# Optimization experiments

Hardware: AMD Instinct MI355X
Metric: run time of the kernel (lower is better)

Reference implementation:

```python
import jax, jax.numpy as jnp
import numpy as np

B, T, D = 2, 1024, 2048      # batch, seq, model dim
E, F, K = 64, 512, 4          # n_experts, expert hidden, top-k
S, HS = 2, 512 * 4            # shared experts, shared hidden = expert_dim * topk


def setup_inputs() -> dict:
    key = jax.random.key(0)
    ks = jax.random.split(key, 9)
    s = 0.02
    f32 = jnp.float32
    return {
        "x": jax.random.normal(ks[0], (B, T, D), f32),
        "router_w": jax.random.normal(ks[1], (D, E), f32) * s,
        "router_bias": jnp.zeros((E,), f32),
        "wg": jax.random.normal(ks[2], (E, D, F), f32) * s,
        "wu": jax.random.normal(ks[3], (E, D, F), f32) * s,
        "wd": jax.random.normal(ks[4], (E, F, D), f32) * s,
        "swg": jax.random.normal(ks[5], (S, D, HS), f32) * s,
        "swu": jax.random.normal(ks[6], (S, D, HS), f32) * s,
        "swd": jax.random.normal(ks[7], (S, HS, D), f32) * s,
    }


def reference(x, router_w, router_bias, wg, wu, wd, swg, swu, swd):
    b, t, d = x.shape
    flat = x.reshape(b * t, d)                      # [N, D]
    n = flat.shape[0]

    # Router: softmax scores, top-k selection on (logits + bias)
    logits = flat @ router_w                         # [N, E]
    scores = jax.nn.softmax(logits, axis=-1)
    _, topk_idx = jax.lax.top_k(logits + router_bias, K)          # [N, K]
    topk_scores = jnp.take_along_axis(scores, topk_idx, axis=-1)  # [N, K]
    topk_scores = topk_scores / topk_scores.sum(axis=-1, keepdims=True)

    # Dense combine weights: w[n, e] = normalized score if expert e selected else 0
    comb = jnp.zeros((n, E), dtype=flat.dtype).at[
        jnp.arange(n)[:, None], topk_idx].set(topk_scores)        # [N, E]

    # Routed experts (SwiGLU), computed densely and masked by combine weights
    g = jax.nn.silu(jnp.einsum('nd,edf->nef', flat, wg))          # [N, E, F]
    u = jnp.einsum('nd,edf->nef', flat, wu)                       # [N, E, F]
    routed = jnp.einsum('ne,nef,efd->nd', comb, g * u, wd)        # [N, D]

    # Shared experts (always active, summed)
    sg = jax.nn.silu(jnp.einsum('nd,sdh->nsh', flat, swg))        # [N, S, HS]
    su = jnp.einsum('nd,sdh->nsh', flat, swu)
    shared = jnp.einsum('nsh,shd->nd', sg * su, swd)              # [N, D]

    return (routed + shared).reshape(b, t, d)
```

## Files before the change

kernel.cpp:

```cpp
#include <hip/hip_runtime.h>
#include <hip/hip_bf16.h>

typedef __bf16 bf16x8 __attribute__((ext_vector_type(8)));
typedef float f32x4 __attribute__((ext_vector_type(4)));
typedef unsigned short u16x4 __attribute__((ext_vector_type(4)));
typedef unsigned short u16x8 __attribute__((ext_vector_type(8)));

#define DEVI __device__ __forceinline__

constexpr int N_TOK = 2048;
constexpr int DIM   = 2048;
constexpr int NEXP  = 64;
constexpr int FDIM  = 512;
constexpr int TOPK  = 4;
constexpr int NSH   = 2;
constexpr int HSH   = 2048;

DEVI unsigned short f2b(float f) {
  union { float fv; unsigned u; } v; v.fv = f;
  unsigned r = v.u + 0x7fffu + ((v.u >> 16) & 1u);
  return (unsigned short)(r >> 16);
}
DEVI float b2f(unsigned short h) {
  union { unsigned u; float f; } v; v.u = ((unsigned)h) << 16;
  return v.f;
}
DEVI void gll16(const void* g, void* l) {
  __builtin_amdgcn_global_load_lds((const __attribute__((address_space(1))) unsigned*)g,
                                   (__attribute__((address_space(3))) unsigned*)l, 16, 0, 0);
}
DEVI unsigned cvtpk(float lo, float hi) {
  unsigned r;
  asm("v_cvt_pk_bf16_f32 %0, %1, %2" : "=v"(r) : "v"(lo), "v"(hi));
  return r;
}
DEVI bf16x8 fragB(const float* base, int str) {
  union { unsigned u[4]; bf16x8 v; } r;
  #pragma unroll
  for (int p = 0; p < 4; ++p) r.u[p] = cvtpk(base[(2 * p) * str], base[(2 * p + 1) * str]);
  return r.v;
}

__global__ void cvt_x_kernel(const float* __restrict__ x, unsigned short* __restrict__ xb) {
  const size_t i = ((size_t)blockIdx.x * 256 + threadIdx.x) * 8;
  const float4 a = *reinterpret_cast<const float4*>(x + i);
  const float4 b = *reinterpret_cast<const float4*>(x + i + 4);
  u16x8 o;
  o[0] = f2b(a.x); o[1] = f2b(a.y); o[2] = f2b(a.z); o[3] = f2b(a.w);
  o[4] = f2b(b.x); o[5] = f2b(b.y); o[6] = f2b(b.z); o[7] = f2b(b.w);
  *reinterpret_cast<u16x8*>(xb + i) = o;
}

__global__ __launch_bounds__(256)
void tr_shared_kernel(const float* __restrict__ swu, const float* __restrict__ swg,
                      const float* __restrict__ swd, unsigned short* __restrict__ swuT,
                      unsigned short* __restrict__ swgT, unsigned short* __restrict__ swdT) {
  __shared__ float Lf[64][68];
  const int tid = threadIdx.x;
  const int r0 = blockIdx.x * 64, c0 = blockIdx.y * 64;
  const int z = blockIdx.z, mat = z >> 1;
  const size_t soff = (size_t)(z & 1) * DIM * HSH;
  const float* in = (mat == 0 ? swu : mat == 1 ? swg : swd) + soff;
  unsigned short* ot = (mat == 0 ? swuT : mat == 1 ? swgT : swdT) + soff;
  #pragma unroll
  for (int j = 0; j < 4; ++j) {
    const int idx = j * 1024 + tid * 4;
    const int row = idx >> 6, col = idx & 63;
    const float4 v = *reinterpret_cast<const float4*>(in + (size_t)(r0 + row) * 2048 + c0 + col);
    *reinterpret_cast<float4*>(&Lf[row][col]) = v;
  }
  __syncthreads();
  #pragma unroll
  for (int j = 0; j < 4; ++j) {
    const int idx = j * 1024 + tid * 4;
    const int orow = idx >> 6, ocol = idx & 63;
    u16x4 o;
    o[0] = f2b(Lf[ocol][orow]);     o[1] = f2b(Lf[ocol + 1][orow]);
    o[2] = f2b(Lf[ocol + 2][orow]); o[3] = f2b(Lf[ocol + 3][orow]);
    *reinterpret_cast<u16x4*>(ot + (size_t)(c0 + orow) * 2048 + r0 + ocol) = o;
  }
}

__global__ __launch_bounds__(256)
void router_kernel(const float* __restrict__ x, const float* __restrict__ rw,
                   const float* __restrict__ rb, int* __restrict__ cnt,
                   int* __restrict__ listTok, float* __restrict__ listW,
                   int* __restrict__ tokEP) {
  __shared__ float Lx[8][128];
  const int tid = threadIdx.x;
  const int lane = tid & 63;
  const int wave = tid >> 6;
  const int tokBase = blockIdx.x * 8;

  float acc0 = 0.f, acc1 = 0.f;
  for (int dc = 0; dc < DIM; dc += 128) {
    __syncthreads();
    {
      const int idx = tid * 4;
      const int row = idx >> 7, col = idx & 127;
      *reinterpret_cast<float4*>(&Lx[row][col]) =
          *reinterpret_cast<const float4*>(x + (size_t)(tokBase + row) * DIM + dc + col);
    }
    __syncthreads();
    #pragma unroll 16
    for (int dd = 0; dd < 128; ++dd) {
      const float r = rw[(size_t)(dc + dd) * NEXP + lane];
      acc0 = fmaf(Lx[wave * 2 + 0][dd], r, acc0);
      acc1 = fmaf(Lx[wave * 2 + 1][dd], r, acc1);
    }
  }

  const float bias = rb[lane];
  #pragma unroll
  for (int t = 0; t < 2; ++t) {
    const float v = (t == 0) ? acc0 : acc1;
    const int token = tokBase + wave * 2 + t;
    float m = v;
    #pragma unroll
    for (int o = 32; o > 0; o >>= 1) m = fmaxf(m, __shfl_xor(m, o));
    const float p = expf(v - m);
    float ss = p;
    #pragma unroll
    for (int o = 32; o > 0; o >>= 1) ss += __shfl_xor(ss, o);
    const float score = p / ss;
    float cur = v + bias;
    float wk[TOPK]; int ik[TOPK]; float wsum = 0.f;
    #pragma unroll
    for (int k = 0; k < TOPK; ++k) {
      float tm = cur;
      #pragma unroll
      for (int o = 32; o > 0; o >>= 1) tm = fmaxf(tm, __shfl_xor(tm, o));
      const unsigned long long msk = __ballot(cur == tm);
      const int sel = (int)__builtin_ctzll(msk);
      const float w = __shfl(score, sel);
      wk[k] = w; ik[k] = sel; wsum += w;
      if (lane == sel) cur = -3.4e38f;
    }
    if (lane < TOPK) {
      const int e = ik[lane];
      const float w = wk[lane] / wsum;
      const int slot = atomicAdd(&cnt[e], 1);
      listTok[(size_t)e * N_TOK + slot] = token;
      listW[(size_t)e * N_TOK + slot] = w;
      tokEP[token * TOPK + lane] = (e << 16) | slot;
    }
  }
}

__global__ void scan_kernel(const int* __restrict__ cnt, int* __restrict__ off) {
  if (threadIdx.x == 0) {
    int s = 0;
    for (int e = 0; e < NEXP; ++e) { off[e] = s; s += cnt[e]; }
  }
}

__global__ __launch_bounds__(256, 4)
void up_shared(const unsigned short* __restrict__ xb,
               const unsigned short* __restrict__ WuT, const unsigned short* __restrict__ WgT,
               unsigned short* __restrict__ H) {
  constexpr int NT = DIM / 64;
  const int tid = threadIdx.x;
  const int f0 = blockIdx.x * 64;
  const int s  = blockIdx.y;
  const int m0 = blockIdx.z * 128;

  __shared__ __align__(16) unsigned short Al[8][128][8];
  __shared__ __align__(16) unsigned short BuL[8][64][8];
  __shared__ __align__(16) unsigned short BgL[8][64][8];

  const int wid = tid >> 6, l = tid & 63;
  const int lc = l & 15, hi = l >> 4;

  const unsigned short* pa0 = xb + (size_t)(m0 + l) * DIM;
  const unsigned short* pa1 = xb + (size_t)(m0 + 64 + l) * DIM;
  const unsigned short* pbu = WuT + (size_t)s * HSH * DIM + (size_t)(f0 + l) * DIM;
  const unsigned short* pbg = WgT + (size_t)s * HSH * DIM + (size_t)(f0 + l) * DIM;

  f32x4 aU[2][4], aG[2][4];
  #pragma unroll
  for (int i = 0; i < 2; ++i)
    #pragma unroll
    for (int j = 0; j < 4; ++j) { aU[i][j] = f32x4{0,0,0,0}; aG[i][j] = f32x4{0,0,0,0}; }

  for (int g = 0; g < NT; ++g) {
    const int d0 = g * 64;
    #pragma unroll
    for (int i = 0; i < 4; ++i) {
      const int idx = wid * 4 + i;
      const int p = idx >> 1, hf = idx & 1;
      gll16((hf ? pa1 : pa0) + d0 + p * 8, &Al[p][hf * 64][0]);
    }
    #pragma unroll
    for (int i = 0; i < 2; ++i) {
      const int p = wid * 2 + i;
      gll16(pbu + d0 + p * 8, &BuL[p][0][0]);
      gll16(pbg + d0 + p * 8, &BgL[p][0][0]);
    }
    __syncthreads();
    #pragma unroll
    for (int ks = 0; ks < 2; ++ks) {
      bf16x8 af[2], bu[4], bg[4];
      #pragma unroll
      for (int mi = 0; mi < 2; ++mi)
        af[mi] = *reinterpret_cast<const bf16x8*>(&Al[ks * 4 + hi][wid * 32 + mi * 16 + lc][0]);
      #pragma unroll
      for (int ni = 0; ni < 4; ++ni) {
        bu[ni] = *reinterpret_cast<const bf16x8*>(&BuL[ks * 4 + hi][ni * 16 + lc][0]);
        bg[ni] = *reinterpret_cast<const bf16x8*>(&BgL[ks * 4 + hi][ni * 16 + lc][0]);
      }
      #pragma unroll
      for (int mi = 0; mi < 2; ++mi)
        #pragma unroll
        for (int ni = 0; ni < 4; ++ni) {
          aU[mi][ni] = __builtin_amdgcn_mfma_f32_16x16x32_bf16(af[mi], bu[ni], aU[mi][ni], 0, 0, 0);
          aG[mi][ni] = __builtin_amdgcn_mfma_f32_16x16x32_bf16(af[mi], bg[ni], aG[mi][ni], 0, 0, 0);
        }
    }
    __syncthreads();
  }

  #pragma unroll
  for (int mi = 0; mi < 2; ++mi)
    #pragma unroll
    for (int ni = 0; ni < 4; ++ni)
      #pragma unroll
      for (int r2 = 0; r2 < 4; ++r2) {
        const int row = wid * 32 + mi * 16 + hi * 4 + r2;
        const int col = f0 + ni * 16 + lc;
        const float g = aG[mi][ni][r2], u = aU[mi][ni][r2];
        H[((size_t)s * N_TOK + m0 + row) * HSH + col] = f2b((g / (1.f + __expf(-g))) * u);
      }
}

__global__ __launch_bounds__(256, 4)
void down_shared(const unsigned short* __restrict__ Hs, const unsigned short* __restrict__ swdT,
                 unsigned short* __restrict__ shP) {
  constexpr int NT = 16;
  const int tid = threadIdx.x;
  const int x0 = blockIdx.x * 128;
  const int kc = blockIdx.y;
  const int m0 = blockIdx.z * 128;
  const int seg = kc >> 1;
  const int kb = (kc & 1) * 1024;

  __shared__ __align__(16) unsigned short Al[8][128][8];
  __shared__ __align__(16) unsigned short Bl[8][128][8];

  const int wid = tid >> 6, l = tid & 63;
  const int lc = l & 15, hi = l >> 4;

  const unsigned short* pa0 = Hs + ((size_t)seg * N_TOK + m0 + l) * HSH + kb;
  const unsigned short* pa1 = Hs + ((size_t)seg * N_TOK + m0 + 64 + l) * HSH + kb;
  const unsigned short* pb0 = swdT + (size_t)seg * HSH * DIM + (size_t)(x0 + l) * HSH + kb;
  const unsigned short* pb1 = swdT + (size_t)seg * HSH * DIM + (size_t)(x0 + 64 + l) * HSH + kb;

  f32x4 acc[2][8];
  #pragma unroll
  for (int i = 0; i < 2; ++i)
    #pragma unroll
    for (int j = 0; j < 8; ++j) acc[i][j] = f32x4{0,0,0,0};

  for (int g = 0; g < NT; ++g) {
    const int d0 = g * 64;
    #pragma unroll
    for (int i = 0; i < 4; ++i) {
      const int idx = wid * 4 + i;
      const int p = idx >> 1, hf = idx & 1;
      gll16((hf ? pa1 : pa0) + d0 + p * 8, &Al[p][hf * 64][0]);
      gll16((hf ? pb1 : pb0) + d0 + p * 8, &Bl[p][hf * 64][0]);
    }
    __syncthreads();
    #pragma unroll
    for (int ks = 0; ks < 2; ++ks) {
      bf16x8 af[2], bq[8];
      #pragma unroll
      for (int mi = 0; mi < 2; ++mi)
        af[mi] = *reinterpret_cast<const bf16x8*>(&Al[ks * 4 + hi][wid * 32 + mi * 16 + lc][0]);
      #pragma unroll
      for (int ni = 0; ni < 8; ++ni)
        bq[ni] = *reinterpret_cast<const bf16x8*>(&Bl[ks * 4 + hi][ni * 16 + lc][0]);
      #pragma unroll
      for (int mi = 0; mi < 2; ++mi)
        #pragma unroll
        for (int ni = 0; ni < 8; ++ni)
          acc[mi][ni] = __builtin_amdgcn_mfma_f32_16x16x32_bf16(af[mi], bq[ni], acc[mi][ni], 0, 0, 0);
    }
    __syncthreads();
  }

  unsigned short* pout = shP + (size_t)kc * N_TOK * DIM;
  #pragma unroll
  for (int mi = 0; mi < 2; ++mi)
    #pragma unroll
    for (int ni = 0; ni < 8; ++ni)
      #pragma unroll
      for (int r2 = 0; r2 < 4; ++r2) {
        const int row = wid * 32 + mi * 16 + hi * 4 + r2;
        const int col = x0 + ni * 16 + lc;
        pout[(size_t)(m0 + row) * DIM + col] = f2b(acc[mi][ni][r2]);
      }
}

__global__ __launch_bounds__(256, 2)
void up_routed(const unsigned short* __restrict__ xb,
               const float* __restrict__ Wu, const float* __restrict__ Wg,
               const int* __restrict__ cnt, const int* __restrict__ off,
               const int* __restrict__ listTok, const float* __restrict__ listW,
               unsigned short* __restrict__ H) {
  constexpr int NT = DIM / 64;
  const int tid = threadIdx.x;
  const int f0 = blockIdx.x * 64;
  const int e  = blockIdx.y;
  const int m0 = blockIdx.z * 256;
  const int c = cnt[e];
  if (m0 >= c) return;
  const int rc = min(256, c - m0);
  const int rowbase = off[e] + m0;

  __shared__ __align__(16) unsigned short Al[8][256][8];
  __shared__ __align__(16) float Bfu[64][64];
  __shared__ __align__(16) float Bfg[64][64];
  __shared__ float wSs[256];

  wSs[tid] = (m0 + tid < c) ? listW[(size_t)e * N_TOK + m0 + tid] : 0.f;

  const int wid = tid >> 6, l = tid & 63;
  const int lc = l & 15, hi = l >> 4;

  const unsigned short* pa[4];
  #pragma unroll
  for (int j = 0; j < 4; ++j) {
    const int tok = listTok[(size_t)e * N_TOK + min(m0 + j * 64 + l, c - 1)];
    pa[j] = xb + (size_t)tok * DIM;
  }
  const float* pwu = Wu + (size_t)e * DIM * FDIM + (size_t)(l >> 4) * FDIM + f0 + (l & 15) * 4;
  const float* pwg = Wg + (size_t)e * DIM * FDIM + (size_t)(l >> 4) * FDIM + f0 + (l & 15) * 4;

  f32x4 aU[4][4], aG[4][4];
  #pragma unroll
  for (int i = 0; i < 4; ++i)
    #pragma unroll
    for (int j = 0; j < 4; ++j) { aU[i][j] = f32x4{0,0,0,0}; aG[i][j] = f32x4{0,0,0,0}; }

  for (int g = 0; g < NT; ++g) {
    const int d0 = g * 64;
    #pragma unroll
    for (int i = 0; i < 8; ++i) {
      const int idx = wid * 8 + i;
      const int p = idx >> 2, j = idx & 3;
      gll16(pa[j] + d0 + p * 8, &Al[p][j * 64][0]);
    }
    #pragma unroll
    for (int i = 0; i < 4; ++i) {
      const int krow = (wid * 4 + i) * 4;
      gll16(pwu + (size_t)(d0 + krow) * FDIM, &Bfu[krow][0]);
      gll16(pwg + (size_t)(d0 + krow) * FDIM, &Bfg[krow][0]);
    }
    __syncthreads();
    #pragma unroll
    for (int ks = 0; ks < 2; ++ks) {
      bf16x8 af[4];
      #pragma unroll
      for (int mi = 0; mi < 4; ++mi)
        af[mi] = *reinterpret_cast<const bf16x8*>(&Al[ks * 4 + hi][wid * 64 + mi * 16 + lc][0]);
      #pragma unroll
      for (int ni = 0; ni < 4; ++ni) {
        const bf16x8 bu = fragB(&Bfu[ks * 32 + hi * 8][ni * 16 + lc], 64);
        const bf16x8 bg = fragB(&Bfg[ks * 32 + hi * 8][ni * 16 + lc], 64);
        #pragma unroll
        for (int mi = 0; mi < 4; ++mi) {
          aU[mi][ni] = __builtin_amdgcn_mfma_f32_16x16x32_bf16(af[mi], bu, aU[mi][ni], 0, 0, 0);
          aG[mi][ni] = __builtin_amdgcn_mfma_f32_16x16x32_bf16(af[mi], bg, aG[mi][ni], 0, 0, 0);
        }
      }
    }
    __syncthreads();
  }

  #pragma unroll
  for (int mi = 0; mi < 4; ++mi)
    #pragma unroll
    for (int ni = 0; ni < 4; ++ni)
      #pragma unroll
      for (int r2 = 0; r2 < 4; ++r2) {
        const int row = wid * 64 + mi * 16 + hi * 4 + r2;
        if (row < rc) {
          const int col = f0 + ni * 16 + lc;
          const float g = aG[mi][ni][r2], u = aU[mi][ni][r2];
          const float h = (g / (1.f + __expf(-g))) * u * wSs[row];
          H[(size_t)(rowbase + row) * FDIM + col] = f2b(h);
        }
      }
}

__global__ __launch_bounds__(256, 2)
void down_routed(const unsigned short* __restrict__ Hr, const float* __restrict__ wd,
                 const int* __restrict__ cnt, const int* __restrict__ off,
                 unsigned short* __restrict__ P) {
  constexpr int NT = FDIM / 64;
  const int tid = threadIdx.x;
  const int x0 = blockIdx.x * 128;
  const int e  = blockIdx.y;
  const int m0 = blockIdx.z * 256;
  const int c = cnt[e];
  if (m0 >= c) return;
  const int rc = min(256, c - m0);
  const int rowbase = off[e] + m0;

  __shared__ __align__(16) unsigned short Al[8][256][8];
  __shared__ __align__(16) float Bf[64][128];

  const int wid = tid >> 6, l = tid & 63;
  const int lc = l & 15, hi = l >> 4;

  const unsigned short* pa[4];
  #pragma unroll
  for (int j = 0; j < 4; ++j)
    pa[j] = Hr + (size_t)(rowbase + min(j * 64 + l, c - m0 - 1)) * FDIM;

  const float* pwd = wd + (size_t)e * FDIM * DIM + (size_t)(l >> 5) * DIM + x0 + (l & 31) * 4;

  f32x4 acc[4][8];
  #pragma unroll
  for (int i = 0; i < 4; ++i)
    #pragma unroll
    for (int j = 0; j < 8; ++j) acc[i][j] = f32x4{0,0,0,0};

  for (int g = 0; g < NT; ++g) {
    const int d0 = g * 64;
    #pragma unroll
    for (int i = 0; i < 8; ++i) {
      const int idx = wid * 8 + i;
      const int p = idx >> 2, j = idx & 3;
      gll16(pa[j] + d0 + p * 8, &Al[p][j * 64][0]);
    }
    #pragma unroll
    for (int i = 0; i < 8; ++i) {
      const int krow = (wid * 8 + i) * 2;
      gll16(pwd + (size_t)(d0 + krow) * DIM, &Bf[krow][0]);
    }
    __syncthreads();
    #pragma unroll
    for (int ks = 0; ks < 2; ++ks) {
      bf16x8 af[4];
      #pragma unroll
      for (int mi = 0; mi < 4; ++mi)
        af[mi] = *reinterpret_cast<const bf16x8*>(&Al[ks * 4 + hi][wid * 64 + mi * 16 + lc][0]);
      #pragma unroll
      for (int ni = 0; ni < 8; ++ni) {
        const bf16x8 bq = fragB(&Bf[ks * 32 + hi * 8][ni * 16 + lc], 128);
        #pragma unroll
        for (int mi = 0; mi < 4; ++mi)
          acc[mi][ni] = __builtin_amdgcn_mfma_f32_16x16x32_bf16(af[mi], bq, acc[mi][ni], 0, 0, 0);
      }
    }
    __syncthreads();
  }

  #pragma unroll
  for (int mi = 0; mi < 4; ++mi)
    #pragma unroll
    for (int ni = 0; ni < 8; ++ni)
      #pragma unroll
      for (int r2 = 0; r2 < 4; ++r2) {
        const int row = wid * 64 + mi * 16 + hi * 4 + r2;
        if (row < rc) {
          const int col = x0 + ni * 16 + lc;
          P[(size_t)(rowbase + row) * DIM + col] = f2b(acc[mi][ni][r2]);
        }
      }
}

__global__ __launch_bounds__(256)
void combine_kernel(const int* __restrict__ tokEP, const int* __restrict__ off,
                    const unsigned short* __restrict__ P, const unsigned short* __restrict__ shP,
                    float* __restrict__ out) {
  const int n = blockIdx.x;
  const int tid = threadIdx.x;
  int rows[4];
  #pragma unroll
  for (int k = 0; k < TOPK; ++k) {
    const int ep = tokEP[n * TOPK + k];
    rows[k] = off[ep >> 16] + (ep & 0xffff);
  }
  const int cc = tid * 8;
  float4 o0 = {0, 0, 0, 0}, o1 = {0, 0, 0, 0};
  #pragma unroll
  for (int k = 0; k < TOPK; ++k) {
    const u16x8 v = *reinterpret_cast<const u16x8*>(P + (size_t)rows[k] * DIM + cc);
    o0.x += b2f(v[0]); o0.y += b2f(v[1]); o0.z += b2f(v[2]); o0.w += b2f(v[3]);
    o1.x += b2f(v[4]); o1.y += b2f(v[5]); o1.z += b2f(v[6]); o1.w += b2f(v[7]);
  }
  #pragma unroll
  for (int j = 0; j < 4; ++j) {
    const u16x8 v = *reinterpret_cast<const u16x8*>(shP + ((size_t)j * N_TOK + n) * DIM + cc);
    o0.x += b2f(v[0]); o0.y += b2f(v[1]); o0.z += b2f(v[2]); o0.w += b2f(v[3]);
    o1.x += b2f(v[4]); o1.y += b2f(v[5]); o1.z += b2f(v[6]); o1.w += b2f(v[7]);
  }
  float* po = out + (size_t)n * DIM + cc;
  *reinterpret_cast<float4*>(po) = o0;
  *reinterpret_cast<float4*>(po + 4) = o1;
}

extern "C" void kernel_launch(void* const* d_in, const int* in_sizes, int n_in,
                              void* d_out, int out_size, void* d_ws, size_t ws_size,
                              hipStream_t stream) {
  const float* x   = (const float*)d_in[0];
  const float* rw  = (const float*)d_in[1];
  const float* rb  = (const float*)d_in[2];
  const float* wg  = (const float*)d_in[3];
  const float* wu  = (const float*)d_in[4];
  const float* wd  = (const float*)d_in[5];
  const float* swg = (const float*)d_in[6];
  const float* swu = (const float*)d_in[7];
  const float* swd = (const float*)d_in[8];
  float* out = (float*)d_out;
  char* ws = (char*)d_ws;

  int* cnt = (int*)ws;
  int* off = (int*)(ws + 256);
  int* tokEP = (int*)(ws + 4096);
  int* listTok = (int*)(ws + 64 * 1024);
  float* listW = (float*)(ws + 576 * 1024);
  unsigned short* xb   = (unsigned short*)(ws + (size_t) 2 * 1024 * 1024);
  unsigned short* Hr   = (unsigned short*)(ws + (size_t)10 * 1024 * 1024);
  unsigned short* Hs   = (unsigned short*)(ws + (size_t)18 * 1024 * 1024);
  unsigned short* swuT = (unsigned short*)(ws + (size_t)34 * 1024 * 1024);
  unsigned short* swgT = (unsigned short*)(ws + (size_t)50 * 1024 * 1024);
  unsigned short* swdT = (unsigned short*)(ws + (size_t)66 * 1024 * 1024);
  unsigned short* P    = (unsigned short*)(ws + (size_t)82 * 1024 * 1024);
  unsigned short* shP  = swuT;

  hipMemsetAsync(cnt, 0, NEXP * sizeof(int), stream);
  cvt_x_kernel<<<(N_TOK * DIM) / (256 * 8), 256, 0, stream>>>(x, xb);
  router_kernel<<<N_TOK / 8, 256, 0, stream>>>(x, rw, rb, cnt, listTok, listW, tokEP);
  scan_kernel<<<1, 64, 0, stream>>>(cnt, off);
  tr_shared_kernel<<<dim3(32, 32, 6), 256, 0, stream>>>(swu, swg, swd, swuT, swgT, swdT);

  up_shared<<<dim3(HSH / 64, NSH, N_TOK / 128), 256, 0, stream>>>(xb, swuT, swgT, Hs);
  up_routed<<<dim3(FDIM / 64, NEXP, 8), 256, 0, stream>>>(xb, wu, wg, cnt, off, listTok, listW, Hr);
  down_shared<<<dim3(DIM / 128, 4, N_TOK / 128), 256, 0, stream>>>(Hs, swdT, shP);
  down_routed<<<dim3(DIM / 128, NEXP, 8), 256, 0, stream>>>(Hr, wd, cnt, off, P);
  combine_kernel<<<N_TOK, 256, 0, stream>>>(tokEP, off, P, shP, out);
}
```

Measured before the change: 576.6 us.

## Drop shared-weight transpose pass; load fp32 weights directly in shared-expert GEMMs

Removes the separate transpose-and-convert kernel for the shared expert weights. The shared up and down GEMMs now stream the original fp32 weights into LDS and convert them to bf16 fragments on the fly with fragB. This avoids one full read, bf16 write and re-read of about 48M weight elements. The cost is twice the global and LDS traffic per B tile, strided scalar LDS reads plus convert instructions in the inner loop, and lower occupancy bounds (3 instead of 4) because the LDS tiles are larger.

```diff
diff --git a/kernel.cpp b/kernel.cpp
--- a/kernel.cpp
+++ b/kernel.cpp
@@ -49,36 +49,6 @@
   o[0] = f2b(a.x); o[1] = f2b(a.y); o[2] = f2b(a.z); o[3] = f2b(a.w);
   o[4] = f2b(b.x); o[5] = f2b(b.y); o[6] = f2b(b.z); o[7] = f2b(b.w);
   *reinterpret_cast<u16x8*>(xb + i) = o;
-}
-
-__global__ __launch_bounds__(256)
-void tr_shared_kernel(const float* __restrict__ swu, const float* __restrict__ swg,
-                      const float* __restrict__ swd, unsigned short* __restrict__ swuT,
-                      unsigned short* __restrict__ swgT, unsigned short* __restrict__ swdT) {
-  __shared__ float Lf[64][68];
-  const int tid = threadIdx.x;
-  const int r0 = blockIdx.x * 64, c0 = blockIdx.y * 64;
-  const int z = blockIdx.z, mat = z >> 1;
-  const size_t soff = (size_t)(z & 1) * DIM * HSH;
-  const float* in = (mat == 0 ? swu : mat == 1 ? swg : swd) + soff;
-  unsigned short* ot = (mat == 0 ? swuT : mat == 1 ? swgT : swdT) + soff;
-  #pragma unroll
-  for (int j = 0; j < 4; ++j) {
-    const int idx = j * 1024 + tid * 4;
-    const int row = idx >> 6, col = idx & 63;
-    const float4 v = *reinterpret_cast<const float4*>(in + (size_t)(r0 + row) * 2048 + c0 + col);
-    *reinterpret_cast<float4*>(&Lf[row][col]) = v;
-  }
-  __syncthreads();
-  #pragma unroll
-  for (int j = 0; j < 4; ++j) {
-    const int idx = j * 1024 + tid * 4;
-    const int orow = idx >> 6, ocol = idx & 63;
-    u16x4 o;
-    o[0] = f2b(Lf[ocol][orow]);     o[1] = f2b(Lf[ocol + 1][orow]);
-    o[2] = f2b(Lf[ocol + 2][orow]); o[3] = f2b(Lf[ocol + 3][orow]);
-    *reinterpret_cast<u16x4*>(ot + (size_t)(c0 + orow) * 2048 + r0 + ocol) = o;
-  }
 }
 
 __global__ __launch_bounds__(256)
@@ -154,9 +124,9 @@
   }
 }
 
-__global__ __launch_bounds__(256, 4)
+__global__ __launch_bounds__(256, 3)
 void up_shared(const unsigned short* __restrict__ xb,
-               const unsigned short* __restrict__ WuT, const unsigned short* __restrict__ WgT,
+               const float* __restrict__ swu, const float* __restrict__ swg,
                unsigned short* __restrict__ H) {
   constexpr int NT = DIM / 64;
   const int tid = threadIdx.x;
@@ -165,16 +135,16 @@
   const int m0 = blockIdx.z * 128;
 
   __shared__ __align__(16) unsigned short Al[8][128][8];
-  __shared__ __align__(16) unsigned short BuL[8][64][8];
-  __shared__ __align__(16) unsigned short BgL[8][64][8];
+  __shared__ __align__(16) float Bfu[64][64];
+  __shared__ __align__(16) float Bfg[64][64];
 
   const int wid = tid >> 6, l = tid & 63;
   const int lc = l & 15, hi = l >> 4;
 
   const unsigned short* pa0 = xb + (size_t)(m0 + l) * DIM;
   const unsigned short* pa1 = xb + (size_t)(m0 + 64 + l) * DIM;
-  const unsigned short* pbu = WuT + (size_t)s * HSH * DIM + (size_t)(f0 + l) * DIM;
-  const unsigned short* pbg = WgT + (size_t)s * HSH * DIM + (size_t)(f0 + l) * DIM;
+  const float* pwu = swu + (size_t)s * DIM * HSH + (size_t)(l >> 4) * HSH + f0 + (l & 15) * 4;
+  const float* pwg = swg + (size_t)s * DIM * HSH + (size_t)(l >> 4) * HSH + f0 + (l & 15) * 4;
 
   f32x4 aU[2][4], aG[2][4];
   #pragma unroll
@@ -191,30 +161,28 @@
       gll16((hf ? pa1 : pa0) + d0 + p * 8, &Al[p][hf * 64][0]);
     }
     #pragma unroll
-    for (int i = 0; i < 2; ++i) {
-      const int p = wid * 2 + i;
-      gll16(pbu + d0 + p * 8, &BuL[p][0][0]);
-      gll16(pbg + d0 + p * 8, &BgL[p][0][0]);
+    for (int i = 0; i < 4; ++i) {
+      const int krow = (wid * 4 + i) * 4;
+      gll16(pwu + (size_t)(d0 + krow) * HSH, &Bfu[krow][0]);
+      gll16(pwg + (size_t)(d0 + krow) * HSH, &Bfg[krow][0]);
     }
     __syncthreads();
     #pragma unroll
     for (int ks = 0; ks < 2; ++ks) {
-      bf16x8 af[2], bu[4], bg[4];
+      bf16x8 af[2];
       #pragma unroll
       for (int mi = 0; mi < 2; ++mi)
         af[mi] = *reinterpret_cast<const bf16x8*>(&Al[ks * 4 + hi][wid * 32 + mi * 16 + lc][0]);
       #pragma unroll
       for (int ni = 0; ni < 4; ++ni) {
-        bu[ni] = *reinterpret_cast<const bf16x8*>(&BuL[ks * 4 + hi][ni * 16 + lc][0]);
-        bg[ni] = *reinterpret_cast<const bf16x8*>(&BgL[ks * 4 + hi][ni * 16 + lc][0]);
-      }
-      #pragma unroll
-      for (int mi = 0; mi < 2; ++mi)
+        const bf16x8 bu = fragB(&Bfu[ks * 32 + hi * 8][ni * 16 + lc], 64);
+        const bf16x8 bg = fragB(&Bfg[ks * 32 + hi * 8][ni * 16 + lc], 64);
         #pragma unroll
-        for (int ni = 0; ni < 4; ++ni) {
-          aU[mi][ni] = __builtin_amdgcn_mfma_f32_16x16x32_bf16(af[mi], bu[ni], aU[mi][ni], 0, 0, 0);
-          aG[mi][ni] = __builtin_amdgcn_mfma_f32_16x16x32_bf16(af[mi], bg[ni], aG[mi][ni], 0, 0, 0);
+        for (int mi = 0; mi < 2; ++mi) {
+          aU[mi][ni] = __builtin_amdgcn_mfma_f32_16x16x32_bf16(af[mi], bu, aU[mi][ni], 0, 0, 0);
+          aG[mi][ni] = __builtin_amdgcn_mfma_f32_16x16x32_bf16(af[mi], bg, aG[mi][ni], 0, 0, 0);
         }
+      }
     }
     __syncthreads();
   }
@@ -232,8 +200,8 @@
       }
 }
 
-__global__ __launch_bounds__(256, 4)
-void down_shared(const unsigned short* __restrict__ Hs, const unsigned short* __restrict__ swdT,
+__global__ __launch_bounds__(256, 3)
+void down_shared(const unsigned short* __restrict__ Hs, const float* __restrict__ swd,
                  unsigned short* __restrict__ shP) {
   constexpr int NT = 16;
   const int tid = threadIdx.x;
@@ -244,15 +212,14 @@
   const int kb = (kc & 1) * 1024;
 
   __shared__ __align__(16) unsigned short Al[8][128][8];
-  __shared__ __align__(16) unsigned short Bl[8][128][8];
+  __shared__ __align__(16) float Bf[64][128];
 
   const int wid = tid >> 6, l = tid & 63;
   const int lc = l & 15, hi = l >> 4;
 
   const unsigned short* pa0 = Hs + ((size_t)seg * N_TOK + m0 + l) * HSH + kb;
   const unsigned short* pa1 = Hs + ((size_t)seg * N_TOK + m0 + 64 + l) * HSH + kb;
-  const unsigned short* pb0 = swdT + (size_t)seg * HSH * DIM + (size_t)(x0 + l) * HSH + kb;
-  const unsigned short* pb1 = swdT + (size_t)seg * HSH * DIM + (size_t)(x0 + 64 + l) * HSH + kb;
+  const float* pwd = swd + (size_t)seg * HSH * DIM + (size_t)(kb + (l >> 5)) * DIM + x0 + (l & 31) * 4;
 
   f32x4 acc[2][8];
   #pragma unroll
@@ -267,23 +234,26 @@
       const int idx = wid * 4 + i;
       const int p = idx >> 1, hf = idx & 1;
       gll16((hf ? pa1 : pa0) + d0 + p * 8, &Al[p][hf * 64][0]);
-      gll16((hf ? pb1 : pb0) + d0 + p * 8, &Bl[p][hf * 64][0]);
+    }
+    #pragma unroll
+    for (int i = 0; i < 8; ++i) {
+      const int krow = (wid * 8 + i) * 2;
+      gll16(pwd + (size_t)(d0 + krow) * DIM, &Bf[krow][0]);
     }
     __syncthreads();
     #pragma unroll
     for (int ks = 0; ks < 2; ++ks) {
-      bf16x8 af[2], bq[8];
+      bf16x8 af[2];
       #pragma unroll
       for (int mi = 0; mi < 2; ++mi)
         af[mi] = *reinterpret_cast<const bf16x8*>(&Al[ks * 4 + hi][wid * 32 + mi * 16 + lc][0]);
       #pragma unroll
-      for (int ni = 0; ni < 8; ++ni)
-        bq[ni] = *reinterpret_cast<const bf16x8*>(&Bl[ks * 4 + hi][ni * 16 + lc][0]);
-      #pragma unroll
-      for (int mi = 0; mi < 2; ++mi)
+      for (int ni = 0; ni < 8; ++ni) {
+        const bf16x8 bq = fragB(&Bf[ks * 32 + hi * 8][ni * 16 + lc], 128);
         #pragma unroll
-        for (int ni = 0; ni < 8; ++ni)
-          acc[mi][ni] = __builtin_amdgcn_mfma_f32_16x16x32_bf16(af[mi], bq[ni], acc[mi][ni], 0, 0, 0);
+        for (int mi = 0; mi < 2; ++mi)
+          acc[mi][ni] = __builtin_amdgcn_mfma_f32_16x16x32_bf16(af[mi], bq, acc[mi][ni], 0, 0, 0);
+      }
     }
     __syncthreads();
   }
@@ -522,24 +492,20 @@
   int* tokEP = (int*)(ws + 4096);
   int* listTok = (int*)(ws + 64 * 1024);
   float* listW = (float*)(ws + 576 * 1024);
-  unsigned short* xb   = (unsigned short*)(ws + (size_t) 2 * 1024 * 1024);
-  unsigned short* Hr   = (unsigned short*)(ws + (size_t)10 * 1024 * 1024);
-  unsigned short* Hs   = (unsigned short*)(ws + (size_t)18 * 1024 * 1024);
-  unsigned short* swuT = (unsigned short*)(ws + (size_t)34 * 1024 * 1024);
-  unsigned short* swgT = (unsigned short*)(ws + (size_t)50 * 1024 * 1024);
-  unsigned short* swdT = (unsigned short*)(ws + (size_t)66 * 1024 * 1024);
-  unsigned short* P    = (unsigned short*)(ws + (size_t)82 * 1024 * 1024);
-  unsigned short* shP  = swuT;
+  unsigned short* xb  = (unsigned short*)(ws + (size_t) 2 * 1024 * 1024);
+  unsigned short* Hr  = (unsigned short*)(ws + (size_t)10 * 1024 * 1024);
+  unsigned short* Hs  = (unsigned short*)(ws + (size_t)18 * 1024 * 1024);
+  unsigned short* P   = (unsigned short*)(ws + (size_t)34 * 1024 * 1024);
+  unsigned short* shP = (unsigned short*)(ws + (size_t)66 * 1024 * 1024);
 
   hipMemsetAsync(cnt, 0, NEXP * sizeof(int), stream);
   cvt_x_kernel<<<(N_TOK * DIM) / (256 * 8), 256, 0, stream>>>(x, xb);
   router_kernel<<<N_TOK / 8, 256, 0, stream>>>(x, rw, rb, cnt, listTok, listW, tokEP);
   scan_kernel<<<1, 64, 0, stream>>>(cnt, off);
-  tr_shared_kernel<<<dim3(32, 32, 6), 256, 0, stream>>>(swu, swg, swd, swuT, swgT, swdT);
-
-  up_shared<<<dim3(HSH / 64, NSH, N_TOK / 128), 256, 0, stream>>>(xb, swuT, swgT, Hs);
+
+  up_shared<<<dim3(HSH / 64, NSH, N_TOK / 128), 256, 0, stream>>>(xb, swu, swg, Hs);
   up_routed<<<dim3(FDIM / 64, NEXP, 8), 256, 0, stream>>>(xb, wu, wg, cnt, off, listTok, listW, Hr);
-  down_shared<<<dim3(DIM / 128, 4, N_TOK / 128), 256, 0, stream>>>(Hs, swdT, shP);
+  down_shared<<<dim3(DIM / 128, 4, N_TOK / 128), 256, 0, stream>>>(Hs, swd, shP);
   down_routed<<<dim3(DIM / 128, NEXP, 8), 256, 0, stream>>>(Hr, wd, cnt, off, P);
   combine_kernel<<<N_TOK, 256, 0, stream>>>(tokEP, off, P, shP, out);
 }
```

Result: slower. 609.3 us (+5.7%).

## Split routed up-projection into two passes and shrink down-projection tiles

Applied to the files above, without the earlier changes.

The fused gate/up routed kernel becomes a templated kernel launched twice. The first pass writes the up projection to H as bf16, and the second computes the gate, reads u back from H and applies SiLU and the routing weight. The down-projection tile narrows from 128 to 64 columns, and both kernels raise launch bounds to 3 blocks per SU to cut accumulator registers and LDS and raise occupancy. In exchange the token gather from x is read twice, H takes an extra bf16 round trip through global memory (the u value is rounded before the product), and there are more blocks and one extra launch.

```diff
diff --git a/kernel.cpp b/kernel.cpp
--- a/kernel.cpp
+++ b/kernel.cpp
@@ -301,9 +301,9 @@
       }
 }
 
-__global__ __launch_bounds__(256, 2)
-void up_routed(const unsigned short* __restrict__ xb,
-               const float* __restrict__ Wu, const float* __restrict__ Wg,
+template<bool GPASS>
+__global__ __launch_bounds__(256, 3)
+void up_routed(const unsigned short* __restrict__ xb, const float* __restrict__ W,
                const int* __restrict__ cnt, const int* __restrict__ off,
                const int* __restrict__ listTok, const float* __restrict__ listW,
                unsigned short* __restrict__ H) {
@@ -318,11 +318,10 @@
   const int rowbase = off[e] + m0;
 
   __shared__ __align__(16) unsigned short Al[8][256][8];
-  __shared__ __align__(16) float Bfu[64][64];
-  __shared__ __align__(16) float Bfg[64][64];
+  __shared__ __align__(16) float Bf[64][64];
   __shared__ float wSs[256];
 
-  wSs[tid] = (m0 + tid < c) ? listW[(size_t)e * N_TOK + m0 + tid] : 0.f;
+  if (GPASS) wSs[tid] = (m0 + tid < c) ? listW[(size_t)e * N_TOK + m0 + tid] : 0.f;
 
   const int wid = tid >> 6, l = tid & 63;
   const int lc = l & 15, hi = l >> 4;
@@ -333,14 +332,13 @@
     const int tok = listTok[(size_t)e * N_TOK + min(m0 + j * 64 + l, c - 1)];
     pa[j] = xb + (size_t)tok * DIM;
   }
-  const float* pwu = Wu + (size_t)e * DIM * FDIM + (size_t)(l >> 4) * FDIM + f0 + (l & 15) * 4;
-  const float* pwg = Wg + (size_t)e * DIM * FDIM + (size_t)(l >> 4) * FDIM + f0 + (l & 15) * 4;
-
-  f32x4 aU[4][4], aG[4][4];
+  const float* pw = W + (size_t)e * DIM * FDIM + (size_t)(l >> 4) * FDIM + f0 + (l & 15) * 4;
+
+  f32x4 acc[4][4];
   #pragma unroll
   for (int i = 0; i < 4; ++i)
     #pragma unroll
-    for (int j = 0; j < 4; ++j) { aU[i][j] = f32x4{0,0,0,0}; aG[i][j] = f32x4{0,0,0,0}; }
+    for (int j = 0; j < 4; ++j) acc[i][j] = f32x4{0,0,0,0};
 
   for (int g = 0; g < NT; ++g) {
     const int d0 = g * 64;
@@ -353,8 +351,7 @@
     #pragma unroll
     for (int i = 0; i < 4; ++i) {
       const int krow = (wid * 4 + i) * 4;
-      gll16(pwu + (size_t)(d0 + krow) * FDIM, &Bfu[krow][0]);
-      gll16(pwg + (size_t)(d0 + krow) * FDIM, &Bfg[krow][0]);
+      gll16(pw + (size_t)(d0 + krow) * FDIM, &Bf[krow][0]);
     }
     __syncthreads();
     #pragma unroll
@@ -365,13 +362,10 @@
         af[mi] = *reinterpret_cast<const bf16x8*>(&Al[ks * 4 + hi][wid * 64 + mi * 16 + lc][0]);
       #pragma unroll
       for (int ni = 0; ni < 4; ++ni) {
-        const bf16x8 bu = fragB(&Bfu[ks * 32 + hi * 8][ni * 16 + lc], 64);
-        const bf16x8 bg = fragB(&Bfg[ks * 32 + hi * 8][ni * 16 + lc], 64);
+        const bf16x8 bq = fragB(&Bf[ks * 32 + hi * 8][ni * 16 + lc], 64);
         #pragma unroll
-        for (int mi = 0; mi < 4; ++mi) {
-          aU[mi][ni] = __builtin_amdgcn_mfma_f32_16x16x32_bf16(af[mi], bu, aU[mi][ni], 0, 0, 0);
-          aG[mi][ni] = __builtin_amdgcn_mfma_f32_16x16x32_bf16(af[mi], bg, aG[mi][ni], 0, 0, 0);
-        }
+        for (int mi = 0; mi < 4; ++mi)
+          acc[mi][ni] = __builtin_amdgcn_mfma_f32_16x16x32_bf16(af[mi], bq, acc[mi][ni], 0, 0, 0);
       }
     }
     __syncthreads();
@@ -386,20 +380,25 @@
         const int row = wid * 64 + mi * 16 + hi * 4 + r2;
         if (row < rc) {
           const int col = f0 + ni * 16 + lc;
-          const float g = aG[mi][ni][r2], u = aU[mi][ni][r2];
-          const float h = (g / (1.f + __expf(-g))) * u * wSs[row];
-          H[(size_t)(rowbase + row) * FDIM + col] = f2b(h);
+          const size_t idx = (size_t)(rowbase + row) * FDIM + col;
+          const float v = acc[mi][ni][r2];
+          if (GPASS) {
+            const float u = b2f(H[idx]);
+            H[idx] = f2b((v / (1.f + __expf(-v))) * u * wSs[row]);
+          } else {
+            H[idx] = f2b(v);
+          }
         }
       }
 }
 
-__global__ __launch_bounds__(256, 2)
+__global__ __launch_bounds__(256, 3)
 void down_routed(const unsigned short* __restrict__ Hr, const float* __restrict__ wd,
                  const int* __restrict__ cnt, const int* __restrict__ off,
                  unsigned short* __restrict__ P) {
   constexpr int NT = FDIM / 64;
   const int tid = threadIdx.x;
-  const int x0 = blockIdx.x * 128;
+  const int x0 = blockIdx.x * 64;
   const int e  = blockIdx.y;
   const int m0 = blockIdx.z * 256;
   const int c = cnt[e];
@@ -408,7 +407,7 @@
   const int rowbase = off[e] + m0;
 
   __shared__ __align__(16) unsigned short Al[8][256][8];
-  __shared__ __align__(16) float Bf[64][128];
+  __shared__ __align__(16) float Bf[64][64];
 
   const int wid = tid >> 6, l = tid & 63;
   const int lc = l & 15, hi = l >> 4;
@@ -418,13 +417,13 @@
   for (int j = 0; j < 4; ++j)
     pa[j] = Hr + (size_t)(rowbase + min(j * 64 + l, c - m0 - 1)) * FDIM;
 
-  const float* pwd = wd + (size_t)e * FDIM * DIM + (size_t)(l >> 5) * DIM + x0 + (l & 31) * 4;
-
-  f32x4 acc[4][8];
+  const float* pwd = wd + (size_t)e * FDIM * DIM + (size_t)(l >> 4) * DIM + x0 + (l & 15) * 4;
+
+  f32x4 acc[4][4];
   #pragma unroll
   for (int i = 0; i < 4; ++i)
     #pragma unroll
-    for (int j = 0; j < 8; ++j) acc[i][j] = f32x4{0,0,0,0};
+    for (int j = 0; j < 4; ++j) acc[i][j] = f32x4{0,0,0,0};
 
   for (int g = 0; g < NT; ++g) {
     const int d0 = g * 64;
@@ -435,8 +434,8 @@
       gll16(pa[j] + d0 + p * 8, &Al[p][j * 64][0]);
     }
     #pragma unroll
-    for (int i = 0; i < 8; ++i) {
-      const int krow = (wid * 8 + i) * 2;
+    for (int i = 0; i < 4; ++i) {
+      const int krow = (wid * 4 + i) * 4;
       gll16(pwd + (size_t)(d0 + krow) * DIM, &Bf[krow][0]);
     }
     __syncthreads();
@@ -447,8 +446,8 @@
       for (int mi = 0; mi < 4; ++mi)
         af[mi] = *reinterpret_cast<const bf16x8*>(&Al[ks * 4 + hi][wid * 64 + mi * 16 + lc][0]);
       #pragma unroll
-      for (int ni = 0; ni < 8; ++ni) {
-        const bf16x8 bq = fragB(&Bf[ks * 32 + hi * 8][ni * 16 + lc], 128);
+      for (int ni = 0; ni < 4; ++ni) {
+        const bf16x8 bq = fragB(&Bf[ks * 32 + hi * 8][ni * 16 + lc], 64);
         #pragma unroll
         for (int mi = 0; mi < 4; ++mi)
           acc[mi][ni] = __builtin_amdgcn_mfma_f32_16x16x32_bf16(af[mi], bq, acc[mi][ni], 0, 0, 0);
@@ -460,7 +459,7 @@
   #pragma unroll
   for (int mi = 0; mi < 4; ++mi)
     #pragma unroll
-    for (int ni = 0; ni < 8; ++ni)
+    for (int ni = 0; ni < 4; ++ni)
       #pragma unroll
       for (int r2 = 0; r2 < 4; ++r2) {
         const int row = wid * 64 + mi * 16 + hi * 4 + r2;
@@ -538,8 +537,9 @@
   tr_shared_kernel<<<dim3(32, 32, 6), 256, 0, stream>>>(swu, swg, swd, swuT, swgT, swdT);
 
   up_shared<<<dim3(HSH / 64, NSH, N_TOK / 128), 256, 0, stream>>>(xb, swuT, swgT, Hs);
-  up_routed<<<dim3(FDIM / 64, NEXP, 8), 256, 0, stream>>>(xb, wu, wg, cnt, off, listTok, listW, Hr);
+  up_routed<false><<<dim3(FDIM / 64, NEXP, 8), 256, 0, stream>>>(xb, wu, cnt, off, listTok, listW, Hr);
+  up_routed<true ><<<dim3(FDIM / 64, NEXP, 8), 256, 0, stream>>>(xb, wg, cnt, off, listTok, listW, Hr);
   down_shared<<<dim3(DIM / 128, 4, N_TOK / 128), 256, 0, stream>>>(Hs, swdT, shP);
-  down_routed<<<dim3(DIM / 128, NEXP, 8), 256, 0, stream>>>(Hr, wd, cnt, off, P);
+  down_routed<<<dim3(DIM / 64, NEXP, 8), 256, 0, stream>>>(Hr, wd, cnt, off, P);
   combine_kernel<<<N_TOK, 256, 0, stream>>>(tokEP, off, P, shP, out);
 }
```

After: 643.3 us. +11.6%, slower.

## Double-buffer LDS staging in routed up-projection kernel with half-depth K tiles

Applied to the files above, without the earlier changes.

The routed gate/up GEMM kernel now uses two LDS buffers of 32-wide K tiles instead of one 64-wide tile. The next tile's global-to-LDS loads are issued before the current tile's MFMAs, so memory latency can overlap with compute. Total shared-memory footprint stays the same. The trade-off is twice as many loop iterations and barriers, and each barrier still waits for the in-flight prefetch, which limits how much overlap is possible.

```diff
diff --git a/kernel.cpp b/kernel.cpp
--- a/kernel.cpp
+++ b/kernel.cpp
@@ -307,7 +307,7 @@
                const int* __restrict__ cnt, const int* __restrict__ off,
                const int* __restrict__ listTok, const float* __restrict__ listW,
                unsigned short* __restrict__ H) {
-  constexpr int NT = DIM / 64;
+  constexpr int NT = DIM / 32;
   const int tid = threadIdx.x;
   const int f0 = blockIdx.x * 64;
   const int e  = blockIdx.y;
@@ -317,9 +317,9 @@
   const int rc = min(256, c - m0);
   const int rowbase = off[e] + m0;
 
-  __shared__ __align__(16) unsigned short Al[8][256][8];
-  __shared__ __align__(16) float Bfu[64][64];
-  __shared__ __align__(16) float Bfg[64][64];
+  __shared__ __align__(16) unsigned short Al[2][4][256][8];
+  __shared__ __align__(16) float Bfu[2][32][64];
+  __shared__ __align__(16) float Bfg[2][32][64];
   __shared__ float wSs[256];
 
   wSs[tid] = (m0 + tid < c) ? listW[(size_t)e * N_TOK + m0 + tid] : 0.f;
@@ -342,36 +342,37 @@
     #pragma unroll
     for (int j = 0; j < 4; ++j) { aU[i][j] = f32x4{0,0,0,0}; aG[i][j] = f32x4{0,0,0,0}; }
 
+  auto stage = [&](int g, int b) {
+    const int d0 = g * 32;
+    #pragma unroll
+    for (int j = 0; j < 4; ++j)
+      gll16(pa[j] + d0 + wid * 8, &Al[b][wid][j * 64][0]);
+    #pragma unroll
+    for (int i = 0; i < 2; ++i) {
+      const int krow = (wid * 2 + i) * 4;
+      gll16(pwu + (size_t)(d0 + krow) * FDIM, &Bfu[b][krow][0]);
+      gll16(pwg + (size_t)(d0 + krow) * FDIM, &Bfg[b][krow][0]);
+    }
+  };
+
+  stage(0, 0);
+  __syncthreads();
+
   for (int g = 0; g < NT; ++g) {
-    const int d0 = g * 64;
-    #pragma unroll
-    for (int i = 0; i < 8; ++i) {
-      const int idx = wid * 8 + i;
-      const int p = idx >> 2, j = idx & 3;
-      gll16(pa[j] + d0 + p * 8, &Al[p][j * 64][0]);
-    }
-    #pragma unroll
-    for (int i = 0; i < 4; ++i) {
-      const int krow = (wid * 4 + i) * 4;
-      gll16(pwu + (size_t)(d0 + krow) * FDIM, &Bfu[krow][0]);
-      gll16(pwg + (size_t)(d0 + krow) * FDIM, &Bfg[krow][0]);
-    }
-    __syncthreads();
-    #pragma unroll
-    for (int ks = 0; ks < 2; ++ks) {
-      bf16x8 af[4];
-      #pragma unroll
-      for (int mi = 0; mi < 4; ++mi)
-        af[mi] = *reinterpret_cast<const bf16x8*>(&Al[ks * 4 + hi][wid * 64 + mi * 16 + lc][0]);
-      #pragma unroll
-      for (int ni = 0; ni < 4; ++ni) {
-        const bf16x8 bu = fragB(&Bfu[ks * 32 + hi * 8][ni * 16 + lc], 64);
-        const bf16x8 bg = fragB(&Bfg[ks * 32 + hi * 8][ni * 16 + lc], 64);
-        #pragma unroll
-        for (int mi = 0; mi < 4; ++mi) {
-          aU[mi][ni] = __builtin_amdgcn_mfma_f32_16x16x32_bf16(af[mi], bu, aU[mi][ni], 0, 0, 0);
-          aG[mi][ni] = __builtin_amdgcn_mfma_f32_16x16x32_bf16(af[mi], bg, aG[mi][ni], 0, 0, 0);
-        }
+    const int b = g & 1;
+    if (g + 1 < NT) stage(g + 1, b ^ 1);
+    bf16x8 af[4];
+    #pragma unroll
+    for (int mi = 0; mi < 4; ++mi)
+      af[mi] = *reinterpret_cast<const bf16x8*>(&Al[b][hi][wid * 64 + mi * 16 + lc][0]);
+    #pragma unroll
+    for (int ni = 0; ni < 4; ++ni) {
+      const bf16x8 bu = fragB(&Bfu[b][hi * 8][ni * 16 + lc], 64);
+      const bf16x8 bg = fragB(&Bfg[b][hi * 8][ni * 16 + lc], 64);
+      #pragma unroll
+      for (int mi = 0; mi < 4; ++mi) {
+        aU[mi][ni] = __builtin_amdgcn_mfma_f32_16x16x32_bf16(af[mi], bu, aU[mi][ni], 0, 0, 0);
+        aG[mi][ni] = __builtin_amdgcn_mfma_f32_16x16x32_bf16(af[mi], bg, aG[mi][ni], 0, 0, 0);
       }
     }
     __syncthreads();
```

New measurement: 611.5 us. 1.06x slower.
